# Optimization experiments

Hardware: AMD Instinct MI355X
Metric: run time of the kernel (lower is better)

The kernel has to match this reference:

```python
import jax, jax.numpy as jnp
import numpy as np

B, N, K, NC, EMB, Z, AD = 16, 2048, 20, 16, 1024, 256, 64

def _lrelu(x):
    return jnp.where(x > 0, x, 0.2 * x)

def _bn(x, g, b, axes):
    # BatchNorm (training-mode batch stats, biased var, eps=1e-5); channel axis = 1
    m = x.mean(axes, keepdims=True)
    v = x.var(axes, keepdims=True)
    sh = [1] * x.ndim; sh[1] = -1
    return (x - m) * jax.lax.rsqrt(v + 1e-5) * g.reshape(sh) + b.reshape(sh)

def _c2(w, x):  # 1x1 Conv2d, no bias
    return jnp.einsum('oc,bcnk->bonk', w, x)

def _c1(w, x):  # 1x1 Conv1d, no bias
    return jnp.einsum('oc,bcn->bon', w, x)

def _knn(x, k):  # x: (B,C,N) -> idx (B,N,k)
    inner = -2.0 * jnp.einsum('bcn,bcm->bnm', x, x)
    xx = jnp.sum(x * x, axis=1)  # (B,N)
    pd = -xx[:, :, None] - inner - xx[:, None, :]  # negative squared dist
    return jax.lax.top_k(pd, k)[1]

def _graph_feat(x, idx):  # x: (B,C,N), idx: (B,N,k) -> (B,2C,N,k)
    xt = x.transpose(0, 2, 1)  # (B,N,C)
    feat = jax.vmap(lambda a, i: a[i])(xt, idx)  # (B,N,k,C)
    xc = jnp.broadcast_to(xt[:, :, None, :], feat.shape)
    return jnp.concatenate([feat - xc, xc], axis=-1).transpose(0, 3, 1, 2)

def setup_inputs():
    key = jax.random.key(0)
    ks = jax.random.split(key, 16)
    rn = lambda k, sh: (jax.random.normal(k, sh) * 0.05).astype(jnp.float32)
    d = {
        'xyz': jax.random.normal(ks[0], (B, N, 3), jnp.float32),
        'flow': jax.random.normal(ks[1], (B, N, 3), jnp.float32),
        'eps': jax.random.normal(ks[2], (B, Z), jnp.float32),
        'w_c1a': rn(ks[3], (60, 6)),   'w_c1b': rn(ks[4], (60, 60)),
        'w_c2a': rn(ks[5], (60, 120)), 'w_c2b': rn(ks[6], (60, 60)),
        'w_c3': rn(ks[7], (EMB, 120)),
        'w_mu': rn(ks[8], (Z, EMB)),  'b_mu': jnp.zeros((Z,), jnp.float32),
        'w_var': rn(ks[9], (Z, EMB)), 'b_var': jnp.zeros((Z,), jnp.float32),
        'w_enc': rn(ks[10], (64, NC)),
        'w_cub1': rn(ks[11], (256, Z + 64)), 'w_cub2': rn(ks[12], (120, 256)),
        'w_q': rn(ks[13], (AD, 120)), 'w_k': rn(ks[14], (AD, 120)),
    }
    for nm, c in [('c1a', 60), ('c1b', 60), ('c2a', 60), ('c2b', 60), ('c3', EMB)]:
        d['g_' + nm] = jnp.ones((c,), jnp.float32)
        d['bb_' + nm] = jnp.zeros((c,), jnp.float32)
    return d

def reference(xyz, flow, eps, w_c1a, w_c1b, w_c2a, w_c2b, w_c3, w_mu, b_mu,
              w_var, b_var, w_enc, w_cub1, w_cub2, w_q, w_k,
              g_c1a, bb_c1a, g_c1b, bb_c1b, g_c2a, bb_c2a, g_c2b, bb_c2b, g_c3, bb_c3):
    x = xyz.transpose(0, 2, 1)  # (B,3,N)
    idx = _knn(x, K)
    h = _graph_feat(x, idx)  # (B,6,N,K)
    h = _lrelu(_bn(_c2(w_c1a, h), g_c1a, bb_c1a, (0, 2, 3)))
    h = _lrelu(_bn(_c2(w_c1b, h), g_c1b, bb_c1b, (0, 2, 3)))
    x1 = h.max(axis=-1)  # (B,60,N)
    h = _graph_feat(x1, idx)  # low_dim_idx=1: reuse xyz knn
    h = _lrelu(_bn(_c2(w_c2a, h), g_c2a, bb_c2a, (0, 2, 3)))
    h = _lrelu(_bn(_c2(w_c2b, h), g_c2b, bb_c2b, (0, 2, 3)))
    x2 = h.max(axis=-1)
    x_per = jnp.concatenate([x1, x2], axis=1)  # (B,120,N)
    g = _lrelu(_bn(_c1(w_c3, x_per), g_c3, bb_c3, (0, 2))).max(axis=-1)  # (B,EMB)
    mu = g @ w_mu.T + b_mu
    log_var = g @ w_var.T + b_var
    z = eps * jnp.exp(0.5 * log_var) + mu  # (B,Z)
    cub = jnp.broadcast_to(jnp.eye(NC, dtype=xyz.dtype), (xyz.shape[0], NC, NC))
    cvec = _lrelu(_c1(w_enc, cub))  # (B,64,NC)
    xc = jnp.concatenate([jnp.broadcast_to(z[:, :, None], (z.shape[0], Z, NC)), cvec], axis=1)
    xc = _lrelu(_c1(w_cub1, xc))
    x_cuboid = _lrelu(_c1(w_cub2, xc))  # (B,120,NC)
    Q = _c1(w_q, x_per) / jnp.sqrt(jnp.float32(AD))  # (B,AD,N)
    Kf = _c1(w_k, x_cuboid)  # (B,AD,NC)
    scores = jnp.einsum('bcm,bcn->bmn', Kf, Q)  # (B,NC,N)
    assign = jax.nn.softmax(scores, axis=1).transpose(0, 2, 1)  # (B,N,NC)
    return (x_per, x_cuboid, z[:, :, None], mu, log_var, assign)
```

## Files before the change

### kernel.cpp

```cpp
#include <hip/hip_runtime.h>

typedef unsigned int u32;
typedef unsigned short u16;

#define BB 16
#define NN 2048
#define KK 20
#define EE (BB*NN*KK)
#define PP (BB*NN)
#define NCHK 8
#define CHKSZ (NN/NCHK)

#define O_XPER 0
#define O_XCUB 3932160
#define O_Z    3962880
#define O_MU   3966976
#define O_LV   3971072
#define O_ASG  3975168

__device__ double g_part[524288];
__device__ double g_std[2560];
__device__ float  g_st[2560];
__device__ float  g_zf[BB*256];
__device__ float  g_Kf[BB*1024];
__device__ u16    g_idx[EE];
__device__ float  g_xpf[(size_t)PP*120];
__device__ float  g_e1[(size_t)EE*60];
__device__ float  g_e2[(size_t)EE*60];

#define S1B_D 128
#define S2A_D 256
#define S2B_D 384
#define S1A_AB 0
#define S1B_AB 128
#define S2A_AB 256
#define S2B_AB 384
#define S3A 512
#define S3B 1536

#define MB_OFF 320000

#define NEG_BIG -1.0e30f

__device__ __forceinline__ float lrelu(float x){ return x > 0.f ? x : 0.2f*x; }

__device__ __forceinline__ void xrow(int bn, int c0, int cnt, float* d){
  const float* s = g_xpf + (size_t)bn*120 + c0;
  #pragma unroll 4
  for (int i=0;i<cnt;i+=4){
    float4 v = *(const float4*)(s+i);
    d[i]=v.x; d[i+1]=v.y; d[i+2]=v.z; d[i+3]=v.w;
  }
}

__device__ __forceinline__ float pdcalc(float4 pm, float qx, float qy, float qz, float qw){
  float dot = fmaf(qx,pm.x, fmaf(qy,pm.y, qz*pm.z));
  float t = fmaf(2.f, dot, -qw);
  return t - pm.w;
}

#define KT_DECL \
  float td0=NEG_BIG,td1=NEG_BIG,td2=NEG_BIG,td3=NEG_BIG,td4=NEG_BIG, \
        td5=NEG_BIG,td6=NEG_BIG,td7=NEG_BIG,td8=NEG_BIG,td9=NEG_BIG, \
        td10=NEG_BIG,td11=NEG_BIG,td12=NEG_BIG,td13=NEG_BIG,td14=NEG_BIG, \
        td15=NEG_BIG,td16=NEG_BIG,td17=NEG_BIG,td18=NEG_BIG,td19=NEG_BIG;
#define KT_CSW(u,l) { float mx = fmaxf(td##u, td##l); float mn = fminf(td##u, td##l); td##u = mx; td##l = mn; }
#define KT_INSERT(pd) \
  if ((pd) > td19){ \
    td19 = (pd); \
    KT_CSW(18,19) KT_CSW(17,18) KT_CSW(16,17) KT_CSW(15,16) \
    KT_CSW(14,15) KT_CSW(13,14) KT_CSW(12,13) KT_CSW(11,12) \
    KT_CSW(10,11) KT_CSW(9,10)  KT_CSW(8,9)   KT_CSW(7,8)   \
    KT_CSW(6,7)   KT_CSW(5,6)   KT_CSW(4,5)   KT_CSW(3,4)   \
    KT_CSW(2,3)   KT_CSW(1,2)   KT_CSW(0,1) }

__global__ __launch_bounds__(128) void k_knnt(const float* __restrict__ xyz){
  __shared__ float4 cand[CHKSZ];
  int qg = blockIdx.x >> 3;
  int c  = blockIdx.x & 7;
  int b  = qg >> 4;
  int n0 = (qg & 15) << 7;
  int t  = threadIdx.x;
  int m0 = c*CHKSZ;
  for (int i=t;i<CHKSZ;i+=128){
    const float* s = xyz + ((size_t)((b<<11)+m0+i))*3;
    float x=s[0], y=s[1], z=s[2];
    cand[i] = make_float4(x,y,z, fmaf(x,x,fmaf(y,y,z*z)));
  }
  __syncthreads();
  int n = n0 + t;
  const float* qs = xyz + ((size_t)((b<<11)+n))*3;
  float qx=qs[0], qy=qs[1], qz=qs[2];
  float qw = fmaf(qx,qx,fmaf(qy,qy,qz*qz));
  KT_DECL
  for (int i=0;i<CHKSZ;i++){
    float pd = pdcalc(cand[i], qx,qy,qz,qw);
    KT_INSERT(pd)
  }
  int p = (b<<11) + n;
  float* outd = g_e1;
  #define KOUT(k) outd[(size_t)(c*KK+k)*PP + p] = td##k;
  KOUT(0) KOUT(1) KOUT(2) KOUT(3) KOUT(4) KOUT(5) KOUT(6) KOUT(7) KOUT(8) KOUT(9)
  KOUT(10) KOUT(11) KOUT(12) KOUT(13) KOUT(14) KOUT(15) KOUT(16) KOUT(17) KOUT(18) KOUT(19)
  #undef KOUT
}

__global__ __launch_bounds__(256) void k_knnu(){
  int q = blockIdx.x*256 + threadIdx.x;
  const float* ind = g_e1;
  KT_DECL
  for (int i=0;i<NCHK*KK;i++){
    float pd = ind[(size_t)i*PP + q];
    KT_INSERT(pd)
  }
  g_e2[q] = td19;
}

__global__ __launch_bounds__(256) void k_knns1(const float* __restrict__ xyz){
  __shared__ float4 cand[CHKSZ];
  int gid = blockIdx.x*256 + threadIdx.x;
  int c = gid >> 15;
  int q = gid & (PP-1);
  int b = q >> 11;
  int t = threadIdx.x;
  for (int i=t;i<CHKSZ;i+=256){
    const float* s = xyz + ((size_t)((b<<11)+c*CHKSZ+i))*3;
    float x=s[0], y=s[1], z=s[2];
    cand[i] = make_float4(x,y,z, fmaf(x,x,fmaf(y,y,z*z)));
  }
  __syncthreads();
  const float* qs = xyz + (size_t)q*3;
  float qx=qs[0], qy=qs[1], qz=qs[2];
  float qw = fmaf(qx,qx,fmaf(qy,qy,qz*qz));
  float T = g_e2[q];
  u32 cgt=0, ceq=0;
  for (int i=0;i<CHKSZ;i++){
    float pd = pdcalc(cand[i], qx,qy,qz,qw);
    cgt += (pd > T) ? 1u : 0u;
    ceq += (pd == T) ? 1u : 0u;
  }
  u32* cntg = (u32*)g_part;
  u32* cnte = cntg + NCHK*PP;
  cntg[c*PP + q] = cgt;
  cnte[c*PP + q] = ceq;
}

__global__ __launch_bounds__(256) void k_knns2(){
  int q = blockIdx.x*256 + threadIdx.x;
  u32* cntg = (u32*)g_part;
  u32* cnte = cntg + NCHK*PP;
  u32* bg   = cnte + NCHK*PP;
  u32* be   = bg   + NCHK*PP;
  u32 acc = 0;
  for (int c=0;c<NCHK;c++){ bg[c*PP+q] = acc; acc += cntg[c*PP+q]; }
  u32 eacc = acc;
  for (int c=0;c<NCHK;c++){ be[c*PP+q] = eacc; eacc += cnte[c*PP+q]; }
}

__global__ __launch_bounds__(256) void k_knns3(const float* __restrict__ xyz){
  __shared__ float4 cand[CHKSZ];
  int gid = blockIdx.x*256 + threadIdx.x;
  int c = gid >> 15;
  int q = gid & (PP-1);
  int b = q >> 11;
  int t = threadIdx.x;
  for (int i=t;i<CHKSZ;i+=256){
    const float* s = xyz + ((size_t)((b<<11)+c*CHKSZ+i))*3;
    float x=s[0], y=s[1], z=s[2];
    cand[i] = make_float4(x,y,z, fmaf(x,x,fmaf(y,y,z*z)));
  }
  __syncthreads();
  const float* qs = xyz + (size_t)q*3;
  float qx=qs[0], qy=qs[1], qz=qs[2];
  float qw = fmaf(qx,qx,fmaf(qy,qy,qz*qz));
  float T = g_e2[q];
  const u32* cntg = (const u32*)g_part;
  const u32* cnte = cntg + NCHK*PP;
  const u32* bg   = cnte + NCHK*PP;
  const u32* be   = bg   + NCHK*PP;
  u32 wgt = bg[c*PP+q];
  u32 weq = be[c*PP+q];
  u16* o = g_idx + (size_t)q*KK;
  for (int i=0;i<CHKSZ;i++){
    float pd = pdcalc(cand[i], qx,qy,qz,qw);
    int m = c*CHKSZ + i;
    if (pd > T && wgt < KK){ o[wgt] = (u16)m; wgt++; }
    else if (pd == T && weq < KK){ o[weq] = (u16)m; weq++; }
  }
}

__global__ __launch_bounds__(256) void k_red60(int dbase, int nblk){
  __shared__ double red[256];
  int s = blockIdx.x;
  int t = threadIdx.x;
  double acc = 0.0;
  for (int i=t;i<nblk;i+=256) acc += g_part[(size_t)i*128 + s];
  red[t] = acc; __syncthreads();
  for (int w=128; w>0; w>>=1){ if (t<w) red[t]+=red[t+w]; __syncthreads(); }
  if (t==0) g_std[dbase+s] = red[0];
}

__global__ __launch_bounds__(64) void k_fin(const float* __restrict__ g, const float* __restrict__ bb,
                                            int dbase, int abase, double invc){
  int c = threadIdx.x;
  if (c < 60){
    double m = g_std[dbase+c]*invc;
    double v = g_std[dbase+64+c]*invc - m*m;
    if (v < 0.0) v = 0.0;
    float r = (float)(1.0/sqrt(v + 1e-5));
    float a = r*g[c];
    g_st[abase+c] = a;
    g_st[abase+64+c] = bb[c] - (float)m*a;
  }
}

__global__ __launch_bounds__(256) void k_gram1(const float* __restrict__ xyz){
  __shared__ double sred[128];
  int tid = threadIdx.x, lane = tid & 63, wv = tid >> 6;
  double acc[27];
  #pragma unroll
  for (int k=0;k<27;k++) acc[k]=0.0;
  for (int it=0; it<8; ++it){
    int edge = (it*320 + blockIdx.x)*256 + tid;
    int row = edge / KK;
    int b = row >> 11;
    int nbr = g_idx[edge];
    const float* cp = xyz + (size_t)row*3;
    const float* np2 = xyz + ((size_t)((b<<11)+nbr))*3;
    float f3=cp[0], f4=cp[1], f5=cp[2];
    float f0=np2[0]-f3, f1=np2[1]-f4, f2=np2[2]-f5;
    float f[6] = {f0,f1,f2,f3,f4,f5};
    #pragma unroll
    for (int i=0;i<6;i++) acc[i] += (double)f[i];
    int k=6;
    #pragma unroll
    for (int i=0;i<6;i++)
      #pragma unroll
      for (int j=i;j<6;j++){ acc[k] += (double)f[i]*(double)f[j]; k++; }
  }
  #pragma unroll
  for (int k=0;k<27;k++){
    double s = acc[k];
    #pragma unroll
    for (int m=1;m<64;m<<=1) s += __shfl_xor(s,m);
    if (lane==0) sred[wv*32+k] = s;
  }
  __syncthreads();
  if (tid < 27)
    g_part[(size_t)blockIdx.x*32 + tid] = sred[tid] + sred[32+tid] + sred[64+tid] + sred[96+tid];
}

__global__ __launch_bounds__(64) void k_fing1(const float* __restrict__ w1a,
                                              const float* __restrict__ gg, const float* __restrict__ bb){
  __shared__ double gsum[27];
  int t = threadIdx.x;
  if (t < 27){
    double s = 0.0;
    for (int i=0;i<320;i++) s += g_part[(size_t)i*32 + t];
    gsum[t] = s;
  }
  __syncthreads();
  if (t < 60){
    float w[6];
    #pragma unroll
    for (int i=0;i<6;i++) w[i] = w1a[t*6+i];
    double S = 0.0;
    #pragma unroll
    for (int i=0;i<6;i++) S += (double)w[i]*gsum[i];
    double Q = 0.0; int k = 6;
    #pragma unroll
    for (int i=0;i<6;i++)
      #pragma unroll
      for (int j=i;j<6;j++){
        double cf = (i==j) ? 1.0 : 2.0;
        Q += cf*(double)w[i]*(double)w[j]*gsum[k]; k++;
      }
    double inv1 = 1.0/(double)EE;
    double m = S*inv1;
    double v = Q*inv1 - m*m;
    if (v < 0.0) v = 0.0;
    float r = (float)(1.0/sqrt(v + 1e-5));
    float A = r*gg[t];
    g_st[S1A_AB+t] = A;
    g_st[S1A_AB+64+t] = bb[t] - (float)m*A;
  }
}

__global__ __launch_bounds__(256) void k_conv1b(const float* __restrict__ xyz,
                                                const float* __restrict__ w1a, const float* __restrict__ w1b){
  __shared__ float ws[360];
  __shared__ float wbs[3600];
  __shared__ float As[60], Bs[60];
  __shared__ double sred[512];
  int tid = threadIdx.x, lane = tid & 63, wv = tid >> 6;
  for (int i=tid;i<360;i+=256) ws[i]=w1a[i];
  for (int i=tid;i<3600;i+=256) wbs[i]=w1b[i];
  if (tid<60){ As[tid]=g_st[S1A_AB+tid]; Bs[tid]=g_st[S1A_AB+64+tid]; }
  __syncthreads();
  int edge = blockIdx.x*256 + tid;
  int row = edge / KK;
  int b = row >> 11;
  int nbr = g_idx[edge];
  const float* cp = xyz + (size_t)row*3;
  const float* np2 = xyz + ((size_t)((b<<11)+nbr))*3;
  float c0=cp[0], c1=cp[1], c2=cp[2];
  float d0=np2[0]-c0, d1=np2[1]-c1, d2=np2[2]-c2;
  float h[60];
  #pragma unroll 4
  for (int o=0;o<60;o++){
    float y = ws[o*6]*d0 + ws[o*6+1]*d1 + ws[o*6+2]*d2 + ws[o*6+3]*c0 + ws[o*6+4]*c1 + ws[o*6+5]*c2;
    h[o] = lrelu(fmaf(As[o], y, Bs[o]));
  }
  const float4* wb4 = (const float4*)wbs;
  double rs=0.0, rq=0.0;
  for (int o=0;o<60;o++){
    float y=0.f;
    #pragma unroll
    for (int c4=0;c4<15;c4++){
      float4 wvv = wb4[o*15+c4];
      y = fmaf(wvv.x, h[c4*4],   y);
      y = fmaf(wvv.y, h[c4*4+1], y);
      y = fmaf(wvv.z, h[c4*4+2], y);
      y = fmaf(wvv.w, h[c4*4+3], y);
    }
    g_e2[(size_t)o*EE + edge] = y;
    float s=y, q=y*y;
    #pragma unroll
    for (int m=1;m<64;m<<=1){ s += __shfl_xor(s,m); q += __shfl_xor(q,m); }
    if (lane==o){ rs += (double)s; rq += (double)q; }
  }
  sred[wv*128 + lane] = rs;
  sred[wv*128 + 64 + lane] = rq;
  __syncthreads();
  if (tid < 128)
    g_part[(size_t)blockIdx.x*128 + tid] = sred[tid] + sred[128+tid] + sred[256+tid] + sred[384+tid];
}

__global__ __launch_bounds__(256) void k_final1s(float* __restrict__ outb){
  int o = blockIdx.x >> 7;
  int bn = ((blockIdx.x & 127) << 8) + threadIdx.x;
  int b = bn >> 11, n = bn & 2047;
  float A = g_st[S1B_AB+o], Bv = g_st[S1B_AB+64+o];
  const float* src = g_e2 + (size_t)o*EE + (size_t)bn*KK;
  float mx = NEG_BIG;
  #pragma unroll
  for (int k=0;k<KK;k++) mx = fmaxf(mx, lrelu(fmaf(A, src[k], Bv)));
  g_xpf[(size_t)bn*120 + o] = mx;
  outb[O_XPER + (size_t)(b*120+o)*NN + n] = mx;
}

__global__ __launch_bounds__(256) void k_pgem2(const float* __restrict__ w2a){
  __shared__ float wd[3600], wcd[3600];
  int tid = threadIdx.x;
  for (int i=tid;i<3600;i+=256){
    int o = i/60, c = i%60;
    float a = w2a[o*120+c], bvl = w2a[o*120+60+c];
    wd[i] = a; wcd[i] = bvl - a;
  }
  __syncthreads();
  int p = blockIdx.x*256 + tid;
  float x[60];
  xrow(p, 0, 60, x);
  float* gU = g_e2;
  float* gV = g_e2 + (size_t)PP*64;
  const float4* wd4  = (const float4*)wd;
  const float4* wcd4 = (const float4*)wcd;
  #pragma unroll 4
  for (int o=0;o<60;o++){
    float u=0.f, v=0.f;
    #pragma unroll
    for (int c4=0;c4<15;c4++){
      float4 a4 = wd4[o*15+c4];
      float4 b4 = wcd4[o*15+c4];
      u = fmaf(a4.x, x[c4*4],   u); v = fmaf(b4.x, x[c4*4],   v);
      u = fmaf(a4.y, x[c4*4+1], u); v = fmaf(b4.y, x[c4*4+1], v);
      u = fmaf(a4.z, x[c4*4+2], u); v = fmaf(b4.z, x[c4*4+2], v);
      u = fmaf(a4.w, x[c4*4+3], u); v = fmaf(b4.w, x[c4*4+3], v);
    }
    gU[(size_t)p*64 + o] = u;
    gV[(size_t)p*64 + o] = v;
  }
}

__global__ __launch_bounds__(256) void k_conv2a(){
  __shared__ double sred[512];
  int tid = threadIdx.x, lane = tid & 63, wv = tid >> 6;
  int edge = blockIdx.x*256 + tid;
  int row = edge / KK;
  int b = row >> 11;
  int nbr = g_idx[edge];
  int pn = (b<<11)+nbr;
  const float4* gU = (const float4*)g_e2;
  const float4* gV = (const float4*)(g_e2 + (size_t)PP*64);
  double rs=0.0, rq=0.0;
  #pragma unroll
  for (int o4=0;o4<15;o4++){
    float4 uu = gU[(size_t)pn*16 + o4];
    float4 vv = gV[(size_t)row*16 + o4];
    float y0=uu.x+vv.x, y1=uu.y+vv.y, y2=uu.z+vv.z, y3=uu.w+vv.w;
    g_e1[(size_t)(o4*4+0)*EE + edge] = y0;
    g_e1[(size_t)(o4*4+1)*EE + edge] = y1;
    g_e1[(size_t)(o4*4+2)*EE + edge] = y2;
    g_e1[(size_t)(o4*4+3)*EE + edge] = y3;
    float ys[4] = {y0,y1,y2,y3};
    #pragma unroll
    for (int j=0;j<4;j++){
      float s=ys[j], q=ys[j]*ys[j];
      #pragma unroll
      for (int m=1;m<64;m<<=1){ s += __shfl_xor(s,m); q += __shfl_xor(q,m); }
      if (lane==o4*4+j){ rs += (double)s; rq += (double)q; }
    }
  }
  sred[wv*128 + lane] = rs;
  sred[wv*128 + 64 + lane] = rq;
  __syncthreads();
  if (tid < 128)
    g_part[(size_t)blockIdx.x*128 + tid] = sred[tid] + sred[128+tid] + sred[256+tid] + sred[384+tid];
}

__global__ __launch_bounds__(256) void k_conv2b(const float* __restrict__ w2b){
  __shared__ float wbs[3600];
  __shared__ float As[60], Bs[60];
  __shared__ double sred[512];
  int tid = threadIdx.x, lane = tid & 63, wv = tid >> 6;
  for (int i=tid;i<3600;i+=256) wbs[i]=w2b[i];
  if (tid<60){ As[tid]=g_st[S2A_AB+tid]; Bs[tid]=g_st[S2A_AB+64+tid]; }
  __syncthreads();
  int edge = blockIdx.x*256 + tid;
  float h[60];
  #pragma unroll 4
  for (int o=0;o<60;o++) h[o] = lrelu(fmaf(As[o], g_e1[(size_t)o*EE + edge], Bs[o]));
  const float4* wb4 = (const float4*)wbs;
  double rs=0.0, rq=0.0;
  for (int o=0;o<60;o++){
    float y=0.f;
    #pragma unroll
    for (int c4=0;c4<15;c4++){
      float4 wvv = wb4[o*15+c4];
      y = fmaf(wvv.x, h[c4*4],   y);
      y = fmaf(wvv.y, h[c4*4+1], y);
      y = fmaf(wvv.z, h[c4*4+2], y);
      y = fmaf(wvv.w, h[c4*4+3], y);
    }
    g_e2[(size_t)o*EE + edge] = y;
    float s=y, q=y*y;
    #pragma unroll
    for (int m=1;m<64;m<<=1){ s += __shfl_xor(s,m); q += __shfl_xor(q,m); }
    if (lane==o){ rs += (double)s; rq += (double)q; }
  }
  sred[wv*128 + lane] = rs;
  sred[wv*128 + 64 + lane] = rq;
  __syncthreads();
  if (tid < 128)
    g_part[(size_t)blockIdx.x*128 + tid] = sred[tid] + sred[128+tid] + sred[256+tid] + sred[384+tid];
}

__global__ __launch_bounds__(256) void k_final2s(float* __restrict__ outb){
  int o = blockIdx.x >> 7;
  int bn = ((blockIdx.x & 127) << 8) + threadIdx.x;
  int b = bn >> 11, n = bn & 2047;
  float A = g_st[S2B_AB+o], Bv = g_st[S2B_AB+64+o];
  const float* src = g_e2 + (size_t)o*EE + (size_t)bn*KK;
  float mx = NEG_BIG;
  #pragma unroll
  for (int k=0;k<KK;k++) mx = fmaxf(mx, lrelu(fmaf(A, src[k], Bv)));
  g_xpf[(size_t)bn*120 + 60 + o] = mx;
  outb[O_XPER + (size_t)(b*120+60+o)*NN + n] = mx;
}

#define W_DECL(i) float4 W##i;
#define W_LOAD(i) W##i = wp[i];
#define W_DOT(i)  { float4 xv = xr4[i]; \
  a0 = fmaf(W##i.x, xv.x, a0); a1 = fmaf(W##i.y, xv.y, a1); \
  a2 = fmaf(W##i.z, xv.z, a2); a3 = fmaf(W##i.w, xv.w, a3); }
#define W_ALL(OP) \
  OP(0) OP(1) OP(2) OP(3) OP(4) OP(5) OP(6) OP(7) OP(8) OP(9) \
  OP(10) OP(11) OP(12) OP(13) OP(14) OP(15) OP(16) OP(17) OP(18) OP(19) \
  OP(20) OP(21) OP(22) OP(23) OP(24) OP(25) OP(26) OP(27) OP(28) OP(29)

__global__ __launch_bounds__(256, 1) void k_max3s2(const float* __restrict__ wc3){
  __shared__ float xt[64*120];
  __shared__ float redA[256], redB[256], redS[256], redQ[256];
  int tid = threadIdx.x;
  int pj = tid>>6, ei = tid&63;
  int ec = blockIdx.x>>6;
  int b  = (blockIdx.x>>2)&15;
  int seg= blockIdx.x&3;
  int e  = ec*64 + ei;
  W_ALL(W_DECL)
  {
    const float4* wp = (const float4*)(wc3 + (size_t)e*120);
    W_ALL(W_LOAD)
  }
  float mx = NEG_BIG, mn = -NEG_BIG, S = 0.f, Q = 0.f;
  for (int tile=0; tile<8; tile++){
    int p0 = b*2048 + seg*512 + tile*64;
    __syncthreads();
    for (int v=tid; v<1920; v+=256){
      int pk = v/30, c4 = v%30;
      ((float4*)xt)[pk*30+c4] = *(const float4*)(g_xpf + (size_t)(p0+pk)*120 + c4*4);
    }
    __syncthreads();
    for (int k=pj*16; k<pj*16+16; k++){
      const float4* xr4 = (const float4*)(xt + k*120);
      float a0=0.f,a1=0.f,a2=0.f,a3=0.f;
      W_ALL(W_DOT)
      float y = (a0+a1)+(a2+a3);
      mx = fmaxf(mx, y);
      mn = fminf(mn, y);
      S += y;
      Q = fmaf(y, y, Q);
    }
  }
  __syncthreads();
  redA[tid]=mx; redB[tid]=mn; redS[tid]=S; redQ[tid]=Q;
  __syncthreads();
  if (pj==0){
    float M  = fmaxf(fmaxf(redA[ei],redA[64+ei]), fmaxf(redA[128+ei],redA[192+ei]));
    float m2 = fminf(fminf(redB[ei],redB[64+ei]), fminf(redB[128+ei],redB[192+ei]));
    float Ss = (redS[ei]+redS[64+ei])+(redS[128+ei]+redS[192+ei]);
    float Qs = (redQ[ei]+redQ[64+ei])+(redQ[128+ei]+redQ[192+ei]);
    float* MB = (float*)(g_part + MB_OFF);
    int slot = (seg*16+b)*1024 + e;
    MB[slot]          = M;
    MB[65536  + slot] = m2;
    MB[131072 + slot] = Ss;
    MB[196608 + slot] = Qs;
  }
}

__global__ __launch_bounds__(64) void k_fin3R(const float* __restrict__ gg, const float* __restrict__ bb){
  int e = blockIdx.x*64 + threadIdx.x;
  const float* MB = (const float*)(g_part + MB_OFF);
  double S=0.0, Q=0.0;
  for (int j=0;j<64;j++){
    S += (double)MB[131072 + j*1024 + e];
    Q += (double)MB[196608 + j*1024 + e];
  }
  double inv3 = 1.0/(double)PP;
  double m = S*inv3;
  double v = Q*inv3 - m*m;
  if (v < 0.0) v = 0.0;
  float r = (float)(1.0/sqrt(v + 1e-5));
  float A = r*gg[e];
  g_st[S3A+e] = A;
  g_st[S3B+e] = bb[e] - (float)m*A;
}

__global__ __launch_bounds__(256) void k_head(const float* __restrict__ eps,
                                              const float* __restrict__ wmu, const float* __restrict__ bmu,
                                              const float* __restrict__ wvar, const float* __restrict__ bvar,
                                              float* __restrict__ outb){
  int b = blockIdx.x, j = threadIdx.x;
  __shared__ float gs[1024];
  const float* MB = (const float*)(g_part + MB_OFF);
  for (int i=j;i<1024;i+=256){
    float A = g_st[S3A+i], B = g_st[S3B+i];
    float M = NEG_BIG, m2 = -NEG_BIG;
    #pragma unroll
    for (int sg=0;sg<4;sg++){
      M  = fmaxf(M,  MB[(sg*16+b)*1024 + i]);
      m2 = fminf(m2, MB[65536 + (sg*16+b)*1024 + i]);
    }
    float y = (A > 0.f) ? M : ((A < 0.f) ? m2 : M);
    gs[i] = lrelu(fmaf(A, y, B));
  }
  __syncthreads();
  float mu = bmu[j], lv = bvar[j];
  const float4* wm = (const float4*)(wmu + (size_t)j*1024);
  const float4* wv = (const float4*)(wvar + (size_t)j*1024);
  #pragma unroll 4
  for (int e=0;e<256;e++){
    float4 a = wm[e], c = wv[e];
    const float* g4 = gs + e*4;
    mu = fmaf(a.x,g4[0], fmaf(a.y,g4[1], fmaf(a.z,g4[2], fmaf(a.w,g4[3], mu))));
    lv = fmaf(c.x,g4[0], fmaf(c.y,g4[1], fmaf(c.z,g4[2], fmaf(c.w,g4[3], lv))));
  }
  float z = fmaf(eps[b*256+j], expf(0.5f*lv), mu);
  g_zf[b*256+j] = z;
  outb[O_MU + b*256 + j] = mu;
  outb[O_LV + b*256 + j] = lv;
  outb[O_Z  + b*256 + j] = z;
}

__global__ __launch_bounds__(256) void k_cuboid(const float* __restrict__ wenc,
                                                const float* __restrict__ wcub1, const float* __restrict__ wcub2,
                                                const float* __restrict__ wk, float* __restrict__ outb){
  int b = blockIdx.x, t = threadIdx.x;
  __shared__ float xc[320*16];
  __shared__ float hh[256*16];
  __shared__ float xq[120*16];
  for (int i=t;i<320*16;i+=256){
    int c = i>>4, m = i&15;
    xc[i] = (c<256) ? g_zf[b*256+c] : lrelu(wenc[(c-256)*16+m]);
  }
  __syncthreads();
  {
    float acc[16];
    #pragma unroll
    for (int m=0;m<16;m++) acc[m]=0.f;
    for (int c=0;c<320;c++){
      float wv = wcub1[(size_t)t*320+c];
      #pragma unroll
      for (int m=0;m<16;m++) acc[m] = fmaf(wv, xc[c*16+m], acc[m]);
    }
    #pragma unroll
    for (int m=0;m<16;m++) hh[t*16+m] = lrelu(acc[m]);
  }
  __syncthreads();
  if (t<120){
    float a2[16];
    #pragma unroll
    for (int m=0;m<16;m++) a2[m]=0.f;
    for (int c=0;c<256;c++){
      float wv = wcub2[(size_t)t*256+c];
      #pragma unroll
      for (int m=0;m<16;m++) a2[m] = fmaf(wv, hh[c*16+m], a2[m]);
    }
    #pragma unroll
    for (int m=0;m<16;m++){
      float v = lrelu(a2[m]);
      xq[t*16+m] = v;
      outb[O_XCUB + b*1920 + t*16 + m] = v;
    }
  }
  __syncthreads();
  if (t<64){
    float a3[16];
    #pragma unroll
    for (int m=0;m<16;m++) a3[m]=0.f;
    for (int c=0;c<120;c++){
      float wv = wk[t*120+c];
      #pragma unroll
      for (int m=0;m<16;m++) a3[m] = fmaf(wv, xq[c*16+m], a3[m]);
    }
    #pragma unroll
    for (int m=0;m<16;m++) g_Kf[b*1024 + t*16 + m] = a3[m];
  }
}

__global__ __launch_bounds__(64) void k_attn(const float* __restrict__ wq, float* __restrict__ outb){
  int p = blockIdx.x*64 + threadIdx.x;
  int b = p >> 11;
  float x[120];
  xrow(p, 0, 120, x);
  float sc[16];
  #pragma unroll
  for (int m=0;m<16;m++) sc[m]=0.f;
  for (int a=0;a<64;a++){
    float q=0.f;
    #pragma unroll
    for (int c=0;c<120;c++) q = fmaf(wq[a*120+c], x[c], q);
    q *= 0.125f;
    const float* kf = g_Kf + b*1024 + a*16;
    #pragma unroll
    for (int m=0;m<16;m++) sc[m] = fmaf(kf[m], q, sc[m]);
  }
  float mx = sc[0];
  #pragma unroll
  for (int m=1;m<16;m++) mx = fmaxf(mx, sc[m]);
  float s=0.f;
  #pragma unroll
  for (int m=0;m<16;m++){ sc[m] = expf(sc[m]-mx); s += sc[m]; }
  float inv = 1.f/s;
  #pragma unroll
  for (int m=0;m<16;m++) outb[O_ASG + (size_t)p*16 + m] = sc[m]*inv;
}

extern "C" void kernel_launch(void* const* d_in, const int* in_sizes, int n_in,
                              void* d_out, int out_size, void* d_ws, size_t ws_size,
                              hipStream_t stream){
  const float* xyz  = (const float*)d_in[0];
  const float* eps  = (const float*)d_in[2];
  const float* w1a  = (const float*)d_in[3];
  const float* w1b  = (const float*)d_in[4];
  const float* w2a  = (const float*)d_in[5];
  const float* w2b  = (const float*)d_in[6];
  const float* wc3  = (const float*)d_in[7];
  const float* wmu  = (const float*)d_in[8];
  const float* bmu  = (const float*)d_in[9];
  const float* wvar = (const float*)d_in[10];
  const float* bvar = (const float*)d_in[11];
  const float* wenc = (const float*)d_in[12];
  const float* wcub1= (const float*)d_in[13];
  const float* wcub2= (const float*)d_in[14];
  const float* wq   = (const float*)d_in[15];
  const float* wk   = (const float*)d_in[16];
  const float* g1a  = (const float*)d_in[17];
  const float* b1a  = (const float*)d_in[18];
  const float* g1b  = (const float*)d_in[19];
  const float* b1b  = (const float*)d_in[20];
  const float* g2a  = (const float*)d_in[21];
  const float* b2a  = (const float*)d_in[22];
  const float* g2b  = (const float*)d_in[23];
  const float* b2b  = (const float*)d_in[24];
  const float* g3   = (const float*)d_in[25];
  const float* b3   = (const float*)d_in[26];
  float* outb = (float*)d_out;

  const double inv1 = 1.0/(double)EE;

  k_knnt<<<2048,128,0,stream>>>(xyz);
  k_knnu<<<128,256,0,stream>>>();
  k_knns1<<<1024,256,0,stream>>>(xyz);
  k_knns2<<<128,256,0,stream>>>();
  k_knns3<<<1024,256,0,stream>>>(xyz);
  k_gram1<<<320,256,0,stream>>>(xyz);
  k_fing1<<<1,64,0,stream>>>(w1a, g1a, b1a);
  k_conv1b<<<2560,256,0,stream>>>(xyz, w1a, w1b);
  k_red60<<<128,256,0,stream>>>(S1B_D, 2560);
  k_fin<<<1,64,0,stream>>>(g1b, b1b, S1B_D, S1B_AB, inv1);
  k_final1s<<<7680,256,0,stream>>>(outb);
  k_pgem2<<<128,256,0,stream>>>(w2a);
  k_conv2a<<<2560,256,0,stream>>>();
  k_red60<<<128,256,0,stream>>>(S2A_D, 2560);
  k_fin<<<1,64,0,stream>>>(g2a, b2a, S2A_D, S2A_AB, inv1);
  k_conv2b<<<2560,256,0,stream>>>(w2b);
  k_red60<<<128,256,0,stream>>>(S2B_D, 2560);
  k_fin<<<1,64,0,stream>>>(g2b, b2b, S2B_D, S2B_AB, inv1);
  k_final2s<<<7680,256,0,stream>>>(outb);
  k_max3s2<<<1024,256,0,stream>>>(wc3);
  k_fin3R<<<16,64,0,stream>>>(g3, b3);
  k_head<<<16,256,0,stream>>>(eps, wmu, bmu, wvar, bvar, outb);
  k_cuboid<<<16,256,0,stream>>>(wenc, wcub1, wcub2, wk, outb);
  k_attn<<<512,64,0,stream>>>(wq, outb);
}
```

Measured before the change: 1.300 ms.

## Split conv3 dot product across half-waves to halve weight registers

The conv3 max/stat kernel now holds only half of each 120-wide weight row per thread, 15 float4 instead of 30. The two 32-lane halves of a wave each compute a partial dot product and combine them with a shuffle. Each wave covers 32 output channels over all 64 points of a tile, so the shared-memory cross-wave reduction goes away. Segments per batch go from 4 to 8, doubling the partial-stat slots and the reads in the finalize and head kernels. The lower register use and dropped launch_bounds minimum are meant to raise occupancy and latency hiding, at the cost of an extra shuffle per point and each lane reading half as much useful data from LDS per load.

```diff
diff --git a/kernel.cpp b/kernel.cpp
--- a/kernel.cpp
+++ b/kernel.cpp
@@ -38,7 +38,10 @@
 #define S3A 512
 #define S3B 1536
 
-#define MB_OFF 320000
+#define P3_MX 0
+#define P3_MN 131072
+#define P3_S  262144
+#define P3_Q  393216
 
 #define NEG_BIG -1.0e30f
 
@@ -468,74 +471,67 @@
   outb[O_XPER + (size_t)(b*120+60+o)*NN + n] = mx;
 }
 
-#define W_DECL(i) float4 W##i;
-#define W_LOAD(i) W##i = wp[i];
-#define W_DOT(i)  { float4 xv = xr4[i]; \
+#define WH_DECL(i) float4 W##i;
+#define WH_LOAD(i) W##i = wp[i];
+#define WH_DOT(i)  { float4 xv = xp[i]; \
   a0 = fmaf(W##i.x, xv.x, a0); a1 = fmaf(W##i.y, xv.y, a1); \
   a2 = fmaf(W##i.z, xv.z, a2); a3 = fmaf(W##i.w, xv.w, a3); }
-#define W_ALL(OP) \
+#define WH_ALL(OP) \
   OP(0) OP(1) OP(2) OP(3) OP(4) OP(5) OP(6) OP(7) OP(8) OP(9) \
-  OP(10) OP(11) OP(12) OP(13) OP(14) OP(15) OP(16) OP(17) OP(18) OP(19) \
-  OP(20) OP(21) OP(22) OP(23) OP(24) OP(25) OP(26) OP(27) OP(28) OP(29)
-
-__global__ __launch_bounds__(256, 1) void k_max3s2(const float* __restrict__ wc3){
+  OP(10) OP(11) OP(12) OP(13) OP(14)
+
+__global__ __launch_bounds__(256) void k_max3s2(const float* __restrict__ wc3){
   __shared__ float xt[64*120];
-  __shared__ float redA[256], redB[256], redS[256], redQ[256];
   int tid = threadIdx.x;
-  int pj = tid>>6, ei = tid&63;
-  int ec = blockIdx.x>>6;
-  int b  = (blockIdx.x>>2)&15;
-  int seg= blockIdx.x&3;
-  int e  = ec*64 + ei;
-  W_ALL(W_DECL)
+  int lane = tid & 63, wv = tid >> 6;
+  int half = lane >> 5;
+  int ec  = blockIdx.x & 7;
+  int b   = (blockIdx.x >> 3) & 15;
+  int seg = blockIdx.x >> 7;
+  int e   = ec*128 + wv*32 + (lane & 31);
+  WH_ALL(WH_DECL)
   {
-    const float4* wp = (const float4*)(wc3 + (size_t)e*120);
-    W_ALL(W_LOAD)
+    const float4* wp = (const float4*)(wc3 + (size_t)e*120 + half*60);
+    WH_ALL(WH_LOAD)
   }
   float mx = NEG_BIG, mn = -NEG_BIG, S = 0.f, Q = 0.f;
-  for (int tile=0; tile<8; tile++){
-    int p0 = b*2048 + seg*512 + tile*64;
+  for (int tile=0; tile<4; tile++){
+    int p0 = b*2048 + seg*256 + tile*64;
     __syncthreads();
     for (int v=tid; v<1920; v+=256){
       int pk = v/30, c4 = v%30;
       ((float4*)xt)[pk*30+c4] = *(const float4*)(g_xpf + (size_t)(p0+pk)*120 + c4*4);
     }
     __syncthreads();
-    for (int k=pj*16; k<pj*16+16; k++){
-      const float4* xr4 = (const float4*)(xt + k*120);
+    for (int k=0;k<64;k++){
+      const float4* xp = (const float4*)(xt + k*120) + half*15;
       float a0=0.f,a1=0.f,a2=0.f,a3=0.f;
-      W_ALL(W_DOT)
-      float y = (a0+a1)+(a2+a3);
+      WH_ALL(WH_DOT)
+      float p = (a0+a1)+(a2+a3);
+      float y = p + __shfl_xor(p, 32);
       mx = fmaxf(mx, y);
       mn = fminf(mn, y);
       S += y;
       Q = fmaf(y, y, Q);
     }
   }
-  __syncthreads();
-  redA[tid]=mx; redB[tid]=mn; redS[tid]=S; redQ[tid]=Q;
-  __syncthreads();
-  if (pj==0){
-    float M  = fmaxf(fmaxf(redA[ei],redA[64+ei]), fmaxf(redA[128+ei],redA[192+ei]));
-    float m2 = fminf(fminf(redB[ei],redB[64+ei]), fminf(redB[128+ei],redB[192+ei]));
-    float Ss = (redS[ei]+redS[64+ei])+(redS[128+ei]+redS[192+ei]);
-    float Qs = (redQ[ei]+redQ[64+ei])+(redQ[128+ei]+redQ[192+ei]);
-    float* MB = (float*)(g_part + MB_OFF);
+  if (half == 0){
+    float* MB = (float*)g_part;
     int slot = (seg*16+b)*1024 + e;
-    MB[slot]          = M;
-    MB[65536  + slot] = m2;
-    MB[131072 + slot] = Ss;
-    MB[196608 + slot] = Qs;
+    MB[P3_MX + slot] = mx;
+    MB[P3_MN + slot] = mn;
+    MB[P3_S  + slot] = S;
+    MB[P3_Q  + slot] = Q;
   }
 }
 
 __global__ __launch_bounds__(64) void k_fin3R(const float* __restrict__ gg, const float* __restrict__ bb){
   int e = blockIdx.x*64 + threadIdx.x;
-  const float* MB = (const float*)(g_part + MB_OFF);
+  const float* MB = (const float*)g_part;
   double S=0.0, Q=0.0;
-  for (int j=0;j<64;j++){
-    S += (double)MB[131072 + j*1024 + e];
-    Q += (double)MB[196608 + j*1024 + e];
+  for (int j=0;j<128;j++){
+    S += (double)MB[P3_S + j*1024 + e];
+    Q += (double)MB[P3_Q + j*1024 + e];
   }
   double inv3 = 1.0/(double)PP;
   double m = S*inv3;
@@ -553,14 +549,14 @@
                                               float* __restrict__ outb){
   int b = blockIdx.x, j = threadIdx.x;
   __shared__ float gs[1024];
-  const float* MB = (const float*)(g_part + MB_OFF);
+  const float* MB = (const float*)g_part;
   for (int i=j;i<1024;i+=256){
     float A = g_st[S3A+i], B = g_st[S3B+i];
     float M = NEG_BIG, m2 = -NEG_BIG;
     #pragma unroll
-    for (int sg=0;sg<4;sg++){
-      M  = fmaxf(M,  MB[(sg*16+b)*1024 + i]);
-      m2 = fminf(m2, MB[65536 + (sg*16+b)*1024 + i]);
+    for (int sg=0;sg<8;sg++){
+      M  = fmaxf(M,  MB[P3_MX + (sg*16+b)*1024 + i]);
+      m2 = fminf(m2, MB[P3_MN + (sg*16+b)*1024 + i]);
     }
     float y = (A > 0.f) ? M : ((A < 0.f) ? m2 : M);
     gs[i] = lrelu(fmaf(A, y, B));
```

After: 1.277 ms. Within noise of the previous version (-1.8%).
